# Kernel optimization log

Measured on AMD Instinct MI355X. Metric: run time of the kernel, lower is better.

Reference implementation:

```python
import jax, jax.numpy as jnp
import numpy as np
from jax import lax


def _dct_basis():
    # 64 separable 2D DCT-II basis filters, shape [64,1,8,8] (OIHW)
    k = 8
    a = np.full(k, np.sqrt(2.0 / k)); a[0] = np.sqrt(1.0 / k)
    u = np.arange(k)[:, None]; xx = np.arange(k)[None, :]
    B = a[:, None] * np.cos((2 * xx + 1) * u * np.pi / (2 * k))  # [u, x]
    basis = np.einsum('ux,vy->uvxy', B, B).reshape(64, 1, k, k)
    return jnp.asarray(basis, dtype=jnp.float32)


def _conv(x, w, b, pad):
    y = lax.conv_general_dilated(x, w, (1, 1), [(pad, pad), (pad, pad)],
                                 dimension_numbers=('NCHW', 'OIHW', 'NCHW'))
    return y + b[None, :, None, None]


def _bn(x, s, b, m, v, eps=1e-5):
    inv = s * lax.rsqrt(v + eps)
    return x * inv[None, :, None, None] + (b - m * inv)[None, :, None, None]


def _mp2(x):
    return lax.reduce_window(x, -jnp.inf, lax.max, (1, 1, 2, 2), (1, 1, 2, 2), 'VALID')


def setup_inputs() -> dict:
    key = jax.random.key(0)
    ks = jax.random.split(key, 32)
    B = 128
    d = {}
    d['x'] = jax.random.normal(ks[0], (B, 1, 256, 256), jnp.float32)
    d['qvectors'] = jax.random.uniform(ks[1], (B, 64), jnp.float32)
    d['dct_basis'] = _dct_basis()
    def w(k, shape, sc=0.02):
        return jax.random.normal(k, shape, jnp.float32) * sc
    # conv stack
    d['conv1a_w'] = w(ks[2], (64, 1, 5, 5));   d['conv1a_b'] = w(ks[3], (64,))
    d['conv1b_w'] = w(ks[4], (64, 64, 5, 5));  d['conv1b_b'] = w(ks[5], (64,))
    d['conv2a_w'] = w(ks[6], (128, 64, 5, 5)); d['conv2a_b'] = w(ks[7], (128,))
    d['conv3a_w'] = w(ks[8], (256, 128, 5, 5)); d['conv3a_b'] = w(ks[9], (256,))
    # batchnorm (eval-mode) params: scale, bias, running_mean, running_var
    for i, (name, c) in enumerate([('bn1a', 64), ('bn1b', 64), ('bn2a', 128), ('bn3a', 256)]):
        kk = jax.random.split(ks[10 + i], 4)
        d[name + '_s'] = 1.0 + w(kk[0], (c,))
        d[name + '_b'] = w(kk[1], (c,))
        d[name + '_m'] = w(kk[2], (c,))
        d[name + '_v'] = jax.random.uniform(kk[3], (c,), jnp.float32, 0.5, 1.5)
    d['fc1_w'] = w(ks[20], (500, 15 * 8 * 256 + 64), 0.01); d['fc1_b'] = w(ks[21], (500,))
    d['fc2_w'] = w(ks[22], (500, 564), 0.01);               d['fc2_b'] = w(ks[23], (500,))
    d['fc3_w'] = w(ks[24], (2, 564), 0.01);                 d['fc3_b'] = w(ks[25], (2,))
    return d


def reference(x, qvectors, dct_basis,
              conv1a_w, conv1a_b, bn1a_s, bn1a_b, bn1a_m, bn1a_v,
              conv1b_w, conv1b_b, bn1b_s, bn1b_b, bn1b_m, bn1b_v,
              conv2a_w, conv2a_b, bn2a_s, bn2a_b, bn2a_m, bn2a_v,
              conv3a_w, conv3a_b, bn3a_s, bn3a_b, bn3a_m, bn3a_v,
              fc1_w, fc1_b, fc2_w, fc2_b, fc3_w, fc3_b):
    gamma = 1e6
    # --- soft-histogram over DCT coefficients (no_grad in the original) ---
    dct = lax.conv_general_dilated(x, dct_basis, (8, 8), 'VALID',
                                   dimension_numbers=('NCHW', 'OIHW', 'NCHW'))  # [B,64,32,32]
    bins = jnp.arange(-60, 61, dtype=jnp.float32)  # 121 bins

    def step(_, b):
        s = jnp.sum(jax.nn.sigmoid(gamma * (dct - b)), axis=(2, 3)) / 1024.0  # [B,64]
        return None, s
    _, feats = lax.scan(step, None, bins)           # [121,B,64]
    feats = jnp.transpose(feats, (1, 0, 2))          # [B,121,64]
    features = feats[:, 0:120, :] - feats[:, 1:121, :]
    features = lax.stop_gradient(features.reshape(-1, 1, 120, 64))

    # --- CNN backbone ---
    h = jax.nn.relu(_bn(_conv(features, conv1a_w, conv1a_b, 2), bn1a_s, bn1a_b, bn1a_m, bn1a_v))
    h = jax.nn.relu(_bn(_conv(h, conv1b_w, conv1b_b, 2), bn1b_s, bn1b_b, bn1b_m, bn1b_v))
    h = _mp2(h)
    h = jax.nn.relu(_bn(_conv(h, conv2a_w, conv2a_b, 2), bn2a_s, bn2a_b, bn2a_m, bn2a_v))
    h = _mp2(h)
    h = jax.nn.relu(_bn(_conv(h, conv3a_w, conv3a_b, 2), bn3a_s, bn3a_b, bn3a_m, bn3a_v))
    h = _mp2(h)                                      # [B,256,15,8]
    h_flat = h.reshape(-1, 15 * 8 * 256)
    h = jnp.concatenate([qvectors, h_flat], axis=1)
    h = jax.nn.relu(h @ fc1_w.T + fc1_b)
    h = jnp.concatenate([qvectors, h], axis=1)
    h = jax.nn.relu(h @ fc2_w.T + fc2_b)
    h = jnp.concatenate([qvectors, h], axis=1)
    return h @ fc3_w.T + fc3_b
```

## Files before the change

### kernel.cpp

```cpp
#include <hip/hip_runtime.h>


typedef _Float16 half8 __attribute__((ext_vector_type(8)));
typedef _Float16 half4 __attribute__((ext_vector_type(4)));
typedef float f32x16 __attribute__((ext_vector_type(16)));

__device__ __forceinline__ void async_copy16(const void* g, void* l) {
  __builtin_amdgcn_global_load_lds(
      (__attribute__((address_space(1))) void*)g,
      (__attribute__((address_space(3))) void*)l, 16, 0, 0);
}

__global__ __launch_bounds__(256) void dct_kernel(const float* __restrict__ x,
                                                  const float* __restrict__ basis,
                                                  float* __restrict__ dct) {
  __shared__ __align__(16) float Bm[64];
  int tid = threadIdx.x;
  if (tid < 64) {
    int u = tid >> 3, xx = tid & 7;
    Bm[tid] = basis[(u * 8) * 64 + xx * 8] * 2.8284271247461903f;
  }
  __syncthreads();
  int gid = blockIdx.x * 256 + tid;
  int b = gid >> 10, blk = gid & 1023;
  int bi = blk >> 5, bj = blk & 31;
  const float* xp = x + (size_t)b * 65536 + (bi * 8) * 256 + bj * 8;
  float X[64];
#pragma unroll
  for (int r = 0; r < 8; ++r) {
    float4 p = *(const float4*)(xp + r * 256);
    float4 q = *(const float4*)(xp + r * 256 + 4);
    X[r * 8 + 0] = p.x; X[r * 8 + 1] = p.y; X[r * 8 + 2] = p.z; X[r * 8 + 3] = p.w;
    X[r * 8 + 4] = q.x; X[r * 8 + 5] = q.y; X[r * 8 + 6] = q.z; X[r * 8 + 7] = q.w;
  }
  float T[64];
#pragma unroll
  for (int u = 0; u < 8; ++u) {
    float t[8] = {0.f, 0.f, 0.f, 0.f, 0.f, 0.f, 0.f, 0.f};
#pragma unroll
    for (int xx = 0; xx < 8; ++xx) {
      float bm = Bm[u * 8 + xx];
#pragma unroll
      for (int y = 0; y < 8; ++y) t[y] += bm * X[xx * 8 + y];
    }
#pragma unroll
    for (int y = 0; y < 8; ++y) T[u * 8 + y] = t[y];
  }
  float* op = dct + (size_t)b * 65536 + bi * 32 + bj;
#pragma unroll
  for (int v = 0; v < 8; ++v) {
    float dc[8] = {0.f, 0.f, 0.f, 0.f, 0.f, 0.f, 0.f, 0.f};
#pragma unroll
    for (int y = 0; y < 8; ++y) {
      float bm = Bm[v * 8 + y];
#pragma unroll
      for (int u = 0; u < 8; ++u) dc[u] += bm * T[u * 8 + y];
    }
#pragma unroll
    for (int u = 0; u < 8; ++u) op[(u * 8 + v) * 1024] = dc[u];
  }
}

__global__ __launch_bounds__(256) void hist_kernel(const float* __restrict__ dct,
                                                   float* __restrict__ feat) {
  __shared__ __align__(16) float h[16 * 121];
  int tid = threadIdx.x;
  for (int i = tid; i < 16 * 121; i += 256) h[i] = 0.f;
  __syncthreads();
  int b = blockIdx.x >> 6, c = blockIdx.x & 63;
  const float* dp = dct + (size_t)(b * 64 + c) * 1024;
  float* hc = h + (tid & 15) * 121;
  float4 v4 = ((const float4*)dp)[tid];
  float vals[4] = {v4.x, v4.y, v4.z, v4.w};
#pragma unroll
  for (int i = 0; i < 4; ++i) {
    float d = vals[i];
    float fl = floorf(d);
    float t0 = d - fl;
    int k = (int)fl + 60;
    if (t0 >= 2e-5f && t0 <= 1.f - 1.2e-4f) {
      if (k >= 0 && k < 120) atomicAdd(hc + k, 1.0f);
    } else {
      float s0 = 1.f / (1.f + expf(-1e6f * t0));
      float s1 = 1.f / (1.f + expf(1e6f * (1.f - t0)));
      if (k >= 1 && k <= 120) atomicAdd(hc + k - 1, 1.f - s0);
      if (k >= 0 && k < 120)  atomicAdd(hc + k, s0 - s1);
      if (k >= -1 && k < 119) atomicAdd(hc + k + 1, s1);
    }
  }
  __syncthreads();
  for (int f = tid; f < 120; f += 256) {
    float s = 0.f;
#pragma unroll
    for (int l = 0; l < 16; ++l) s += h[l * 121 + f];
    feat[((size_t)b * 120 + f) * 64 + c] = s * (1.f / 1024.f);
  }
}

template <int CI, int CO>
__global__ __launch_bounds__(256) void wtrans(const float* __restrict__ w,
                                              _Float16* __restrict__ wt) {
  int i = blockIdx.x * 256 + threadIdx.x;
  if (i >= (CI / 8) * 26 * CO * 8) return;
  int c8 = i & 7;
  int t = i >> 3;
  int co = t % CO; t /= CO;
  int k = t % 26;
  int cg = t / 26;
  int ci = cg * 8 + c8;
  float v = (k < 25) ? w[((size_t)co * CI + ci) * 25 + k] : 0.f;
  wt[i] = (_Float16)v;
}

__global__ __launch_bounds__(256) void bnprep(const float* __restrict__ cb,
                                              const float* __restrict__ s,
                                              const float* __restrict__ b,
                                              const float* __restrict__ m,
                                              const float* __restrict__ v,
                                              float* __restrict__ scale,
                                              float* __restrict__ shift, int n) {
  int i = threadIdx.x;
  if (i < n) {
    float inv = s[i] * rsqrtf(v[i] + 1e-5f);
    scale[i] = inv;
    shift[i] = (cb[i] - m[i]) * inv + b[i];
  }
}

__global__ __launch_bounds__(256) void conv1a_f16(
    const float* __restrict__ in, const float* __restrict__ wts,
    const float* __restrict__ cb, const float* __restrict__ s_,
    const float* __restrict__ b_, const float* __restrict__ m_,
    const float* __restrict__ v_, _Float16* __restrict__ out) {
  __shared__ __align__(16) float wl[5 * 8 * 20];
  __shared__ __align__(16) float il[12 * 68];
  int tid = threadIdx.x, bid = blockIdx.x;
  int img = bid / 30;
  int r = bid % 30;
  int cob = r / 15;
  int h0 = (r % 15) * 8;
  int cog = tid & 7, wg = (tid >> 3) & 3, hh = tid >> 5;
  float acc[4][16];
#pragma unroll
  for (int i = 0; i < 4; ++i)
#pragma unroll
    for (int j = 0; j < 16; ++j) acc[i][j] = 0.f;
  for (int idx = tid; idx < 32 * 25; idx += 256) {
    int rr = idx % 25, co = idx / 25;
    float v = wts[(cob * 32 + co) * 25 + rr];
    int kh = rr / 5, kw = rr % 5;
    wl[(kh * 8 + (co >> 2)) * 20 + (co & 3) * 5 + kw] = v;
  }
  for (int idx = tid; idx < 12 * 68; idx += 256) {
    int cc = idx % 68, rr = idx / 68;
    int hy = h0 + rr - 2, wx = cc - 2;
    float v = 0.f;
    if (hy >= 0 && hy < 120 && wx >= 0 && wx < 64)
      v = in[(size_t)img * 7680 + hy * 64 + wx];
    il[idx] = v;
  }
  __syncthreads();
#pragma unroll
  for (int kh = 0; kh < 5; ++kh) {
    const float* ir = &il[(hh + kh) * 68 + wg * 16];
    float iv[20];
#pragma unroll
    for (int i = 0; i < 5; ++i) {
      float4 p = *(const float4*)(ir + i * 4);
      iv[i * 4] = p.x; iv[i * 4 + 1] = p.y; iv[i * 4 + 2] = p.z; iv[i * 4 + 3] = p.w;
    }
    const float* wr = &wl[(kh * 8 + cog) * 20];
    float wv[20];
#pragma unroll
    for (int i = 0; i < 5; ++i) {
      float4 p = *(const float4*)(wr + i * 4);
      wv[i * 4] = p.x; wv[i * 4 + 1] = p.y; wv[i * 4 + 2] = p.z; wv[i * 4 + 3] = p.w;
    }
#pragma unroll
    for (int co = 0; co < 4; ++co)
#pragma unroll
      for (int kw = 0; kw < 5; ++kw) {
        float w1 = wv[co * 5 + kw];
#pragma unroll
        for (int w = 0; w < 16; ++w) acc[co][w] += w1 * iv[w + kw];
      }
  }
  int h = h0 + hh;
  int co0 = cob * 32 + cog * 4;
  float inv[4], bia[4];
#pragma unroll
  for (int i = 0; i < 4; ++i) {
    int c = co0 + i;
    inv[i] = s_[c] * rsqrtf(v_[c] + 1e-5f);
    bia[i] = (cb[c] - m_[c]) * inv[i] + b_[c];
  }
  int g = co0 >> 3, off = co0 & 7;
  _Float16* op = out + (((size_t)(img * 8 + g) * 120 + h) * 64) * 8 + off;
#pragma unroll
  for (int w = 0; w < 16; ++w) {
    half4 o;
#pragma unroll
    for (int i = 0; i < 4; ++i)
      o[i] = (_Float16)fmaxf(acc[i][w] * inv[i] + bia[i], 0.f);
    *(half4*)&op[(size_t)(wg * 16 + w) * 8] = o;
  }
}

template <int CI, int CO, int H, int W, int BLK_M, bool OUT_NCHW, bool DBUF>
__global__ __launch_bounds__(512) void conv5_mfma(
    const _Float16* __restrict__ in, const _Float16* __restrict__ wt,
    const float* __restrict__ scale, const float* __restrict__ shift,
    _Float16* __restrict__ out) {
  constexpr int NW_M = BLK_M / 64;
  constexpr int NW_N = 8 / NW_M;
  constexpr int BLK_N = NW_N * 128;
  constexpr int ROWS = BLK_N / W;
  constexpr int TB = (H + ROWS - 1) / ROWS;
  constexpr int NCOB = CO / BLK_M;
  constexpr int HR = ROWS + 4;
  constexpr int HC = W + 4;
  constexpr int CIG = CI / 8;
  constexpr int OH = H / 2, OW = W / 2;
  constexpr int AITER = (HR * HC + 511) / 512;
  constexpr int WBYTES = 26 * BLK_M * 16;
  constexpr int WITER = (WBYTES + 8191) / 8192;
  constexpr int NBUF = DBUF ? 2 : 1;
  constexpr int ASZ = HR * HC * 8;
  constexpr int WSZ = 26 * BLK_M * 8;
  __shared__ __align__(16) _Float16 Alds[NBUF][ASZ];
  __shared__ __align__(16) _Float16 Wlds[NBUF][WSZ];

  int tid = threadIdx.x;
  int bid = blockIdx.x;
  int img = bid / (TB * NCOB);
  int r = bid % (TB * NCOB);
  int tb = r / NCOB;
  int cob = r % NCOB;
  int h0 = tb * ROWS;

  int wid = tid >> 6, l = tid & 63, lo = l & 31, hi = l >> 5;
  int widM = wid / NW_N, widN = wid % NW_N;

  int wbase[2];
#pragma unroll
  for (int mi = 0; mi < 2; ++mi)
    wbase[mi] = (hi * BLK_M + widM * 64 + mi * 32 + lo) * 8;
  int bbase[4];
#pragma unroll
  for (int j = 0; j < 4; ++j) {
    int pix = widN * 128 + j * 32 + lo;
    bbase[j] = ((pix / W) * HC + (pix % W)) * 8;
  }

  f32x16 acc[2][4];
#pragma unroll
  for (int mi = 0; mi < 2; ++mi)
#pragma unroll
    for (int j = 0; j < 4; ++j) acc[mi][j] = (f32x16){};

  auto loadA = [&](int cg, half8* areg) {
    const _Float16* ing = in + (size_t)(img * CIG + cg) * H * W * 8;
#pragma unroll
    for (int it = 0; it < AITER; ++it) {
      int i = tid + it * 512;
      half8 v = {};
      if (i < HR * HC) {
        int rr = i / HC, cc = i % HC;
        int hy = h0 + rr - 2, wx = cc - 2;
        if (hy >= 0 && hy < H && wx >= 0 && wx < W)
          v = *(const half8*)&ing[(size_t)(hy * W + wx) * 8];
      }
      areg[it] = v;
    }
  };
  auto issueW = [&](int cg, int buf) {
    const char* wsrc = (const char*)(wt + ((size_t)cg * 26 * CO + cob * BLK_M) * 8);
#pragma unroll
    for (int rr = 0; rr < WITER; ++rr) {
      int f = rr * 8192 + tid * 16;
      if (f < WBYTES) {
        int row = f / (BLK_M * 16);
        int off = f % (BLK_M * 16);
        async_copy16(wsrc + (size_t)row * (CO * 16) + off,
                     (char*)&Wlds[buf][0] + (rr * 8192 + wid * 1024));
      }
    }
  };
  auto writeA = [&](int buf, half8* areg) {
#pragma unroll
    for (int it = 0; it < AITER; ++it) {
      int i = tid + it * 512;
      if (i < HR * HC) *(half8*)&Alds[buf][i * 8] = areg[it];
    }
  };
  auto compute = [&](int buf) {
#pragma unroll
    for (int p = 0; p < 13; ++p) {
      int pos1 = 2 * p + 1;
      int off0 = ((2 * p) / 5) * HC + ((2 * p) % 5);
      int off1 = (pos1 < 25) ? (pos1 / 5) * HC + (pos1 % 5) : 0;
      int off = (hi ? off1 : off0) * 8;
      half8 af[2], bf[4];
#pragma unroll
      for (int mi = 0; mi < 2; ++mi)
        af[mi] = *(const half8*)&Wlds[buf][wbase[mi] + 2 * p * BLK_M * 8];
#pragma unroll
      for (int j = 0; j < 4; ++j)
        bf[j] = *(const half8*)&Alds[buf][bbase[j] + off];
#pragma unroll
      for (int mi = 0; mi < 2; ++mi)
#pragma unroll
        for (int j = 0; j < 4; ++j)
          acc[mi][j] = __builtin_amdgcn_mfma_f32_32x32x16_f16(
              af[mi], bf[j], acc[mi][j], 0, 0, 0);
    }
  };

  if constexpr (DBUF) {
    half8 areg[AITER];
    loadA(0, areg);
    issueW(0, 0);
    writeA(0, areg);
    __syncthreads();
#pragma unroll 1
    for (int cg = 0; cg < CIG; ++cg) {
      int cur = cg & 1;
      if (cg + 1 < CIG) {
        loadA(cg + 1, areg);
        issueW(cg + 1, cur ^ 1);
      }
      compute(cur);
      if (cg + 1 < CIG) writeA(cur ^ 1, areg);
      __syncthreads();
    }
  } else {
#pragma unroll 1
    for (int cg = 0; cg < CIG; ++cg) {
      half8 areg[AITER];
      loadA(cg, areg);
      issueW(cg, 0);
      writeA(0, areg);
      __syncthreads();
      compute(0);
      __syncthreads();
    }
  }

  if (!OUT_NCHW) {
    constexpr int CGO = CO / 8;
    int gbase = (cob * BLK_M + widM * 64) >> 3;
    bool lane_ok = ((lo & 1) == 0);
#pragma unroll
    for (int mi = 0; mi < 2; ++mi) {
#pragma unroll
      for (int r4 = 0; r4 < 4; ++r4) {
        int g = gbase + mi * 4 + r4;
        int co0 = g * 8 + hi * 4;
        float4 sv = *(const float4*)&scale[co0];
        float4 tv = *(const float4*)&shift[co0];
        float sa[4] = {sv.x, sv.y, sv.z, sv.w};
        float ta[4] = {tv.x, tv.y, tv.z, tv.w};
#pragma unroll
        for (int p = 0; p < 2; ++p) {
          int ja = (W == 64) ? p : 2 * p;
          int jb = (W == 64) ? p + 2 : 2 * p + 1;
          int orow = (W == 64) ? (h0 >> 1) + widN : (h0 >> 1) + widN * 2 + p;
          int ocol = (W == 64) ? p * 16 + (lo >> 1) : (lo >> 1);
          half4 o;
#pragma unroll
          for (int c = 0; c < 4; ++c) {
            int reg = r4 * 4 + c;
            float v0 = fmaxf(acc[mi][ja][reg] * sa[c] + ta[c], 0.f);
            float v1 = fmaxf(acc[mi][jb][reg] * sa[c] + ta[c], 0.f);
            float m = fmaxf(v0, v1);
            m = fmaxf(m, __shfl_xor(m, 1, 64));
            o[c] = (_Float16)m;
          }
          if (lane_ok && orow < OH)
            *(half4*)&out[(((size_t)(img * CGO + g) * OH + orow) * OW + ocol) * 8 +
                          hi * 4] = o;
        }
      }
    }
  } else {
    bool lane_ok = ((lo & 1) == 0) && (lo < 16);
#pragma unroll
    for (int mi = 0; mi < 2; ++mi) {
#pragma unroll
      for (int reg = 0; reg < 16; ++reg) {
        int co = cob * BLK_M + widM * 64 + mi * 32 + (reg & 3) + 8 * (reg >> 2) + 4 * hi;
        float s = scale[co], t = shift[co];
#pragma unroll
        for (int j = 0; j < 4; ++j) {
          float v = fmaxf(acc[mi][j][reg] * s + t, 0.f);
          float m = fmaxf(v, __shfl_xor(v, 16, 64));
          m = fmaxf(m, __shfl_xor(m, 1, 64));
          int orow = (h0 >> 1) + widN * 4 + j;
          if (lane_ok && orow < OH)
            out[((size_t)(img * CO + co) * OH + orow) * OW + ((lo & 15) >> 1)] =
                (_Float16)m;
        }
      }
    }
  }
}

__global__ __launch_bounds__(256, 2) void fc1_mfma(const float* __restrict__ qv,
                                                   const _Float16* __restrict__ p3,
                                                   const float* __restrict__ w,
                                                   float* __restrict__ part) {
  __shared__ __align__(16) _Float16 Wl[8 * 256 * 8];
  __shared__ __align__(16) _Float16 Bl[8 * 128 * 8];
  int tid = threadIdx.x;
  int ks = blockIdx.x >> 1, mt = blockIdx.x & 1;
  int wid = tid >> 6, l = tid & 63, lo = l & 31, hi = l >> 5;
  f32x16 acc[2][4];
#pragma unroll
  for (int mi = 0; mi < 2; ++mi)
#pragma unroll
    for (int j = 0; j < 4; ++j) acc[mi][j] = (f32x16){};

#pragma unroll 1
  for (int i3 = 0; i3 < 3; ++i3) {
    int c = ks + 240 * i3;
    if (c > 480) break;
    for (int idx = tid; idx < 2048; idx += 256) {
      int n_loc = idx >> 3, k8 = idx & 7;
      int n = mt * 256 + n_loc;
      half8 v = {};
      if (n < 500) {
        const float* src = w + (size_t)n * 30784 + c * 64 + k8 * 8;
        float4 f0 = *(const float4*)src;
        float4 f1 = *(const float4*)(src + 4);
        v[0] = (_Float16)f0.x; v[1] = (_Float16)f0.y;
        v[2] = (_Float16)f0.z; v[3] = (_Float16)f0.w;
        v[4] = (_Float16)f1.x; v[5] = (_Float16)f1.y;
        v[6] = (_Float16)f1.z; v[7] = (_Float16)f1.w;
      }
      *(half8*)&Wl[(size_t)(k8 * 256 + n_loc) * 8] = v;
    }
    for (int idx = tid; idx < 1024; idx += 256) {
      int img = idx >> 3, k8 = idx & 7;
      half8 v;
      if (c == 0) {
        const float* src = qv + img * 64 + k8 * 8;
        float4 f0 = *(const float4*)src;
        float4 f1 = *(const float4*)(src + 4);
        v[0] = (_Float16)f0.x; v[1] = (_Float16)f0.y;
        v[2] = (_Float16)f0.z; v[3] = (_Float16)f0.w;
        v[4] = (_Float16)f1.x; v[5] = (_Float16)f1.y;
        v[6] = (_Float16)f1.z; v[7] = (_Float16)f1.w;
      } else {
        v = *(const half8*)&p3[(size_t)img * 30720 + (c * 64 - 64) + k8 * 8];
      }
      *(half8*)&Bl[(size_t)(k8 * 128 + img) * 8] = v;
    }
    __syncthreads();
#pragma unroll
    for (int ks16 = 0; ks16 < 4; ++ks16) {
      half8 af[2], bf[4];
#pragma unroll
      for (int mi = 0; mi < 2; ++mi)
        af[mi] = *(const half8*)&Wl[(size_t)((ks16 * 2 + hi) * 256 + wid * 64 +
                                             mi * 32 + lo) * 8];
#pragma unroll
      for (int j = 0; j < 4; ++j)
        bf[j] = *(const half8*)&Bl[(size_t)((ks16 * 2 + hi) * 128 + j * 32 + lo) * 8];
#pragma unroll
      for (int mi = 0; mi < 2; ++mi)
#pragma unroll
        for (int j = 0; j < 4; ++j)
          acc[mi][j] = __builtin_amdgcn_mfma_f32_32x32x16_f16(
              af[mi], bf[j], acc[mi][j], 0, 0, 0);
    }
    __syncthreads();
  }
#pragma unroll
  for (int mi = 0; mi < 2; ++mi)
#pragma unroll
    for (int reg = 0; reg < 16; ++reg) {
      int n = mt * 256 + wid * 64 + mi * 32 + (reg & 3) + 8 * (reg >> 2) + 4 * hi;
#pragma unroll
      for (int j = 0; j < 4; ++j)
        part[((size_t)ks * 512 + n) * 128 + j * 32 + lo] = acc[mi][j][reg];
    }
}

__global__ __launch_bounds__(256) void fc1_reduce(const float* __restrict__ part,
                                                  const float* __restrict__ bias,
                                                  float* __restrict__ out) {
  int idx = blockIdx.x * 256 + threadIdx.x;
  int img = idx & 127, n = idx >> 7;
  float s = 0.f;
#pragma unroll 8
  for (int ks = 0; ks < 240; ++ks) s += part[((size_t)ks * 512 + n) * 128 + img];
  out[n * 128 + img] = (n < 500) ? fmaxf(s + bias[n], 0.f) : 0.f;
}

__global__ __launch_bounds__(256) void fc2_kernel(const float* __restrict__ qv,
                                                  const float* __restrict__ fc1o,
                                                  const float* __restrict__ w,
                                                  const float* __restrict__ bias,
                                                  float* __restrict__ out) {
  int idx = blockIdx.x * 256 + threadIdx.x;
  if (idx >= 128 * 500) return;
  int m = idx & 127, n = idx >> 7;
  const float* wr = w + (size_t)n * 564;
  float acc = 0.f;
#pragma unroll 8
  for (int k = 0; k < 64; ++k) acc += qv[m * 64 + k] * wr[k];
#pragma unroll 4
  for (int k = 0; k < 500; ++k) acc += fc1o[k * 128 + m] * wr[64 + k];
  out[n * 128 + m] = fmaxf(acc + bias[n], 0.f);
}

__global__ __launch_bounds__(256) void fc3_kernel(const float* __restrict__ qv,
                                                  const float* __restrict__ fc2o,
                                                  const float* __restrict__ w,
                                                  const float* __restrict__ bias,
                                                  float* __restrict__ out) {
  int tid = threadIdx.x;
  int m = tid >> 1, n = tid & 1;
  const float* wr = w + (size_t)n * 564;
  float acc = 0.f;
#pragma unroll 8
  for (int k = 0; k < 64; ++k) acc += qv[m * 64 + k] * wr[k];
#pragma unroll 4
  for (int k = 0; k < 500; ++k) acc += fc2o[k * 128 + m] * wr[64 + k];
  out[m * 2 + n] = acc + bias[n];
}

extern "C" void kernel_launch(void* const* d_in, const int* in_sizes, int n_in,
                              void* d_out, int out_size, void* d_ws, size_t ws_size,
                              hipStream_t stream) {
  (void)in_sizes; (void)n_in; (void)out_size; (void)ws_size;
  const float* x      = (const float*)d_in[0];
  const float* qv     = (const float*)d_in[1];
  const float* basis  = (const float*)d_in[2];
  const float* c1aw   = (const float*)d_in[3];
  const float* c1ab   = (const float*)d_in[4];
  const float* c1bw   = (const float*)d_in[5];
  const float* c1bb   = (const float*)d_in[6];
  const float* c2aw   = (const float*)d_in[7];
  const float* c2ab   = (const float*)d_in[8];
  const float* c3aw   = (const float*)d_in[9];
  const float* c3ab   = (const float*)d_in[10];
  const float* bn1a_s = (const float*)d_in[11];
  const float* bn1a_b = (const float*)d_in[12];
  const float* bn1a_m = (const float*)d_in[13];
  const float* bn1a_v = (const float*)d_in[14];
  const float* bn1b_s = (const float*)d_in[15];
  const float* bn1b_b = (const float*)d_in[16];
  const float* bn1b_m = (const float*)d_in[17];
  const float* bn1b_v = (const float*)d_in[18];
  const float* bn2a_s = (const float*)d_in[19];
  const float* bn2a_b = (const float*)d_in[20];
  const float* bn2a_m = (const float*)d_in[21];
  const float* bn2a_v = (const float*)d_in[22];
  const float* bn3a_s = (const float*)d_in[23];
  const float* bn3a_b = (const float*)d_in[24];
  const float* bn3a_m = (const float*)d_in[25];
  const float* bn3a_v = (const float*)d_in[26];
  const float* fc1w   = (const float*)d_in[27];
  const float* fc1b   = (const float*)d_in[28];
  const float* fc2w   = (const float*)d_in[29];
  const float* fc2b   = (const float*)d_in[30];
  const float* fc3w   = (const float*)d_in[31];
  const float* fc3b   = (const float*)d_in[32];

  float* ws = (float*)d_ws;
  float* feat = ws;
  _Float16* wt1b = (_Float16*)(ws + 1000000);
  _Float16* wt2a = (_Float16*)(ws + 1070000);
  _Float16* wt3a = (_Float16*)(ws + 1200000);
  float* sc1b = ws + 1700000; float* sh1b = ws + 1700100;
  float* sc2a = ws + 1700200; float* sh2a = ws + 1700400;
  float* sc3a = ws + 1700600; float* sh3a = ws + 1701000;
  _Float16* p1 = (_Float16*)(ws + 1710000);
  float* S = ws + 9600000;
  float* dct     = S;
  _Float16* a1c  = (_Float16*)S;
  _Float16* p2   = (_Float16*)(ws + 25400000);
  _Float16* p3   = (_Float16*)(ws + 1710000);
  float* f1p  = S;
  float* f1o  = ws + 29400000;
  float* f2o  = ws + 29500000;

  wtrans<64, 64><<<416, 256, 0, stream>>>(c1bw, wt1b);
  wtrans<64, 128><<<832, 256, 0, stream>>>(c2aw, wt2a);
  wtrans<128, 256><<<3328, 256, 0, stream>>>(c3aw, wt3a);
  bnprep<<<1, 256, 0, stream>>>(c1bb, bn1b_s, bn1b_b, bn1b_m, bn1b_v, sc1b, sh1b, 64);
  bnprep<<<1, 256, 0, stream>>>(c2ab, bn2a_s, bn2a_b, bn2a_m, bn2a_v, sc2a, sh2a, 128);
  bnprep<<<1, 256, 0, stream>>>(c3ab, bn3a_s, bn3a_b, bn3a_m, bn3a_v, sc3a, sh3a, 256);

  dct_kernel<<<512, 256, 0, stream>>>(x, basis, dct);
  hist_kernel<<<128 * 64, 256, 0, stream>>>(dct, feat);

  for (int c = 0; c < 2; ++c) {
    const float* fin = feat + (size_t)c * 64 * 120 * 64;
    _Float16* pout = p1 + (size_t)c * 64 * 8 * 60 * 32 * 8;
    conv1a_f16<<<64 * 30, 256, 0, stream>>>(fin, c1aw, c1ab, bn1a_s, bn1a_b,
                                            bn1a_m, bn1a_v, a1c);
    conv5_mfma<64, 64, 120, 64, 64, false, false><<<64 * 8, 512, 0, stream>>>(
        a1c, wt1b, sc1b, sh1b, pout);
  }

  conv5_mfma<64, 128, 60, 32, 128, false, false><<<128 * 4, 512, 0, stream>>>(
      p1, wt2a, sc2a, sh2a, p2);

  conv5_mfma<128, 256, 30, 16, 128, true, true><<<128 * 2, 512, 0, stream>>>(
      p2, wt3a, sc3a, sh3a, p3);

  fc1_mfma<<<480, 256, 0, stream>>>(qv, p3, fc1w, f1p);
  fc1_reduce<<<256, 256, 0, stream>>>(f1p, fc1b, f1o);
  fc2_kernel<<<250, 256, 0, stream>>>(qv, f1o, fc2w, fc2b, f2o);
  fc3_kernel<<<1, 256, 0, stream>>>(qv, f2o, fc3w, fc3b, (float*)d_out);
}
```

Before: 781.3 us.

## Pad LDS activation rows, stagger per-wave tap order, add MFMA priority

Pads the activation halo tile row pitch from W+4 to W+5 so LDS reads across rows land on different banks. Each wave now starts its walk over the 13 tap pairs at a different offset, using a runtime non-unrolled loop, so waves do not hit the same LDS addresses at the same time. s_setprio is raised around the MFMA block, and conv3a switches from double-buffered to single-buffered LDS. The rolled loop adds runtime index arithmetic and may lose instruction scheduling freedom, and dropping double buffering removes overlap of loads with compute for conv3a.

```diff
diff --git a/kernel.cpp b/kernel.cpp
--- a/kernel.cpp
+++ b/kernel.cpp
@@ -218,14 +218,14 @@
   constexpr int TB = (H + ROWS - 1) / ROWS;
   constexpr int NCOB = CO / BLK_M;
   constexpr int HR = ROWS + 4;
-  constexpr int HC = W + 4;
+  constexpr int HCP = W + 5;
   constexpr int CIG = CI / 8;
   constexpr int OH = H / 2, OW = W / 2;
-  constexpr int AITER = (HR * HC + 511) / 512;
+  constexpr int AITER = (HR * HCP + 511) / 512;
   constexpr int WBYTES = 26 * BLK_M * 16;
   constexpr int WITER = (WBYTES + 8191) / 8192;
   constexpr int NBUF = DBUF ? 2 : 1;
-  constexpr int ASZ = HR * HC * 8;
+  constexpr int ASZ = HR * HCP * 8;
   constexpr int WSZ = 26 * BLK_M * 8;
   __shared__ __align__(16) _Float16 Alds[NBUF][ASZ];
   __shared__ __align__(16) _Float16 Wlds[NBUF][WSZ];
@@ -245,11 +245,11 @@
 #pragma unroll
   for (int mi = 0; mi < 2; ++mi)
     wbase[mi] = (hi * BLK_M + widM * 64 + mi * 32 + lo) * 8;
-  int bbase[4];
+  int blin[4];
 #pragma unroll
   for (int j = 0; j < 4; ++j) {
     int pix = widN * 128 + j * 32 + lo;
-    bbase[j] = ((pix / W) * HC + (pix % W)) * 8;
+    blin[j] = (pix / W) * HCP + (pix % W);
   }
 
   f32x16 acc[2][4];
@@ -264,8 +264,8 @@
     for (int it = 0; it < AITER; ++it) {
       int i = tid + it * 512;
       half8 v = {};
-      if (i < HR * HC) {
-        int rr = i / HC, cc = i % HC;
+      if (i < HR * HCP) {
+        int rr = i / HCP, cc = i % HCP;
         int hy = h0 + rr - 2, wx = cc - 2;
         if (hy >= 0 && hy < H && wx >= 0 && wx < W)
           v = *(const half8*)&ing[(size_t)(hy * W + wx) * 8];
@@ -290,29 +290,42 @@
 #pragma unroll
     for (int it = 0; it < AITER; ++it) {
       int i = tid + it * 512;
-      if (i < HR * HC) *(half8*)&Alds[buf][i * 8] = areg[it];
+      if (i < HR * HCP) *(half8*)&Alds[buf][i * 8] = areg[it];
     }
   };
   auto compute = [&](int buf) {
-#pragma unroll
-    for (int p = 0; p < 13; ++p) {
-      int pos1 = 2 * p + 1;
-      int off0 = ((2 * p) / 5) * HC + ((2 * p) % 5);
-      int off1 = (pos1 < 25) ? (pos1 / 5) * HC + (pos1 % 5) : 0;
-      int off = (hi ? off1 : off0) * 8;
+    int p0 = (wid * 5) % 13;
+    int mypos = 2 * p0 + hi;
+    int kwv = mypos % 5;
+    int loff = (mypos / 5) * HCP + kwv;
+    if (mypos >= 25) { kwv = 0; loff = 0; }
+    int afoff = (2 * p0) * BLK_M * 8;
+    int pcur = p0;
+#pragma unroll 1
+    for (int ps = 0; ps < 13; ++ps) {
       half8 af[2], bf[4];
 #pragma unroll
       for (int mi = 0; mi < 2; ++mi)
-        af[mi] = *(const half8*)&Wlds[buf][wbase[mi] + 2 * p * BLK_M * 8];
+        af[mi] = *(const half8*)&Wlds[buf][wbase[mi] + afoff];
 #pragma unroll
       for (int j = 0; j < 4; ++j)
-        bf[j] = *(const half8*)&Alds[buf][bbase[j] + off];
+        bf[j] = *(const half8*)&Alds[buf][(blin[j] + loff) * 8];
+      __builtin_amdgcn_s_setprio(1);
 #pragma unroll
       for (int mi = 0; mi < 2; ++mi)
 #pragma unroll
         for (int j = 0; j < 4; ++j)
           acc[mi][j] = __builtin_amdgcn_mfma_f32_32x32x16_f16(
               af[mi], bf[j], acc[mi][j], 0, 0, 0);
+      __builtin_amdgcn_s_setprio(0);
+      ++pcur;
+      kwv += 2;
+      bool w5 = kwv >= 5;
+      kwv = w5 ? kwv - 5 : kwv;
+      loff += w5 ? (HCP - 3) : 2;
+      if (loff >= 5 * HCP) loff = 0;
+      afoff += 2 * BLK_M * 8;
+      if (pcur == 13) { pcur = 0; kwv = hi; loff = hi; afoff = 0; }
     }
   };
 
@@ -608,7 +621,7 @@
   conv5_mfma<64, 128, 60, 32, 128, false, false><<<128 * 4, 512, 0, stream>>>(
       p1, wt2a, sc2a, sh2a, p2);
 
-  conv5_mfma<128, 256, 30, 16, 128, true, true><<<128 * 2, 512, 0, stream>>>(
+  conv5_mfma<128, 256, 30, 16, 128, true, false><<<128 * 2, 512, 0, stream>>>(
       p2, wt3a, sc3a, sh3a, p3);
 
   fc1_mfma<<<480, 256, 0, stream>>>(qv, p3, fc1w, f1p);
```

Measured after the change: 826.8 us. +5.8%, slower.
